# Kernel optimization log

Hardware: AMD Instinct MI355X
Metric: run time of the kernel (lower is better)

## Reference

```python
import jax, jax.numpy as jnp
import numpy as np

RCUT = 6.0
EPS = 1e-6
NUM_BASIS = 8
P = 6  # PolynomialSmooth envelope power
N_NODES = 100000
N_EDGES = 3200000
N_GRAPHS = 16

# 27 periodic image shifts: all integer combos of [-1,0,1]^3
_PERIODIC = jnp.asarray(
    np.stack(np.meshgrid(*([[-1, 0, 1]] * 3), indexing='ij'), -1).reshape(27, 3).astype(np.float32)
)


def _sh_lmax2(u):
    """e3nn spherical harmonics, lmax=2, normalize=True, normalization='component'.
    u: [E,3] unit vectors -> [E,9]."""
    x, y, z = u[..., 0], u[..., 1], u[..., 2]
    s3 = jnp.sqrt(jnp.asarray(3.0, u.dtype))
    s5 = jnp.sqrt(jnp.asarray(5.0, u.dtype))
    s15 = jnp.sqrt(jnp.asarray(15.0, u.dtype))
    return jnp.stack([
        jnp.ones_like(x),                      # l=0
        s3 * x, s3 * y, s3 * z,                # l=1
        s15 * x * z,                           # l=2
        s15 * x * y,
        s5 * (y * y - 0.5 * (x * x + z * z)),
        s15 * y * z,
        0.5 * s15 * (z * z - x * x),
    ], axis=-1)


def _bessel(lengths):
    # lengths: [E,1] -> [E,NUM_BASIS]
    k = jnp.arange(1, NUM_BASIS + 1, dtype=lengths.dtype) * jnp.pi / RCUT
    safe = jnp.clip(lengths, EPS, RCUT)
    return jnp.sin(safe * k) / (2.0 * safe)


def _poly_smooth(lengths):
    # standard polynomial envelope (DimeNet-style), zero at r=rcut
    x = jnp.clip(lengths / RCUT, 0.0, 1.0)
    c1 = (P + 1) * (P + 2) / 2.0
    c2 = float(P * (P + 2))
    c3 = P * (P + 1) / 2.0
    xp = x ** P
    return 1.0 - c1 * xp + c2 * xp * x - c3 * xp * x * x


def setup_inputs() -> dict:
    key = jax.random.key(0)
    k1, k2, k3, k4, k5 = jax.random.split(key, 5)
    pos = jax.random.normal(k1, (N_NODES, 3), dtype=jnp.float32) * 5.0
    cells = jax.random.normal(k2, (N_GRAPHS, 3, 3), dtype=jnp.float32)
    edge_index = jax.random.randint(k3, (2, N_EDGES), 0, N_NODES)
    periodic_index = jax.random.randint(k4, (N_EDGES,), 0, 27)
    batch = jnp.sort(jax.random.randint(k5, (N_NODES,), 0, N_GRAPHS))
    return {"pos": pos, "cells": cells, "edge_index": edge_index,
            "periodic_index": periodic_index, "batch": batch}


def reference(pos, cells, edge_index, periodic_index, batch):
    node_src, node_dst = edge_index[0], edge_index[1]
    vectors = pos[node_dst] - pos[node_src]                     # [E,3]
    shifts = _PERIODIC[periodic_index]                          # [E,3]
    src_cells = cells[batch[node_src]]                          # [E,3,3]
    vectors = vectors - jnp.einsum('eij,ei->ej', src_cells, shifts)
    vectors = -vectors                                          # dst == 'atom'
    lengths = jnp.linalg.norm(vectors, axis=-1, keepdims=True)  # [E,1]
    unit = vectors / jnp.maximum(lengths, EPS)                  # normalize=True
    attr = _sh_lmax2(unit)                                      # [E,9]
    basis = _bessel(lengths)                                    # [E,8]
    cutoff = _poly_smooth(lengths)                              # [E,1]
    basis_weight = basis * cutoff                               # [E,8]
    # pack (length, sh attr, smooth, basis_weight) -> [E,19]
    return jnp.concatenate([lengths, attr, cutoff, basis_weight], axis=-1)
```

## Files before the change

### kernel.cpp

```cpp
#include <hip/hip_runtime.h>

#define BLOCK 256
#define EPT 4
#define TILE (BLOCK * EPT)

typedef float vf4 __attribute__((ext_vector_type(4)));

extern "C" __global__ void __launch_bounds__(BLOCK) pack_pos_batch(
    const float* __restrict__ pos,
    const int*  __restrict__ batch,
    vf4* __restrict__ pos4,
    int N)
{
    const int i = blockIdx.x * BLOCK + threadIdx.x;
    if (i < N) {
        vf4 v;
        v.x = pos[3 * i + 0];
        v.y = pos[3 * i + 1];
        v.z = pos[3 * i + 2];
        v.w = __int_as_float(batch[i]);
        pos4[i] = v;
    }
}

template <bool PACKED>
__global__ void __launch_bounds__(BLOCK) edge_encoding_kernel(
    const float* __restrict__ pos,
    const vf4*   __restrict__ pos4,
    const float* __restrict__ cells,
    const int*   __restrict__ eidx,
    const int*   __restrict__ pidx,
    const int*   __restrict__ batch,
    float* __restrict__ out,
    int E)
{
    __shared__ vf4 s_t[16 * 27];
    __shared__ __align__(16) float s_out[BLOCK * 19];

    const int tid = threadIdx.x;
    for (int c = tid; c < 16 * 27; c += BLOCK) {
        const int g = c / 27, p = c % 27;
        const float f0 = (float)(p / 9 - 1);
        const float f1 = (float)((p / 3) % 3 - 1);
        const float f2 = (float)(p % 3 - 1);
        const float* C = cells + g * 9;
        vf4 t;
        t.x = C[0]*f0 + C[3]*f1 + C[6]*f2;
        t.y = C[1]*f0 + C[4]*f1 + C[7]*f2;
        t.z = C[2]*f0 + C[5]*f1 + C[8]*f2;
        t.w = 0.0f;
        s_t[c] = t;
    }
    __syncthreads();

    const long long b0 = (long long)blockIdx.x * TILE;

    int src[EPT], dst[EPT], pp[EPT];
    #pragma unroll
    for (int r = 0; r < EPT; ++r) {
        long long e = b0 + (long long)r * BLOCK + tid;
        if (e >= E) e = E - 1;
        src[r] = __builtin_nontemporal_load(eidx + e);
        dst[r] = __builtin_nontemporal_load(eidx + E + e);
        pp[r]  = __builtin_nontemporal_load(pidx + e);
    }
    vf4 ps[EPT], pd[EPT];
    #pragma unroll
    for (int r = 0; r < EPT; ++r) {
        if (PACKED) {
            ps[r] = pos4[src[r]];
            pd[r] = pos4[dst[r]];
        } else {
            const int s = src[r], d = dst[r];
            ps[r].x = pos[3*s+0]; ps[r].y = pos[3*s+1]; ps[r].z = pos[3*s+2];
            ps[r].w = __int_as_float(batch[s]);
            pd[r].x = pos[3*d+0]; pd[r].y = pos[3*d+1]; pd[r].z = pos[3*d+2];
            pd[r].w = 0.0f;
        }
    }

    const float s3  = 1.7320508075688772f;
    const float s5  = 2.2360679774997896f;
    const float s15 = 3.872983346207417f;

    #pragma unroll
    for (int c = 0; c < EPT; ++c) {
        float row[19];
        {
            const int g = __float_as_int(ps[c].w);
            const vf4 t = s_t[g * 27 + pp[c]];

            const float vx = ps[c].x - pd[c].x + t.x;
            const float vy = ps[c].y - pd[c].y + t.y;
            const float vz = ps[c].z - pd[c].z + t.z;

            const float len  = sqrtf(vx*vx + vy*vy + vz*vz);
            const float invl = __builtin_amdgcn_rcpf(fmaxf(len, 1e-6f));
            const float x = vx * invl, y = vy * invl, z = vz * invl;

            row[0] = len;
            row[1] = 1.0f;
            row[2] = s3 * x;
            row[3] = s3 * y;
            row[4] = s3 * z;
            row[5] = s15 * x * z;
            row[6] = s15 * x * y;
            row[7] = s5  * (y*y - 0.5f*(x*x + z*z));
            row[8] = s15 * y * z;
            row[9] = 0.5f * s15 * (z*z - x*x);

            const float xc = fminf(len * (1.0f/6.0f), 1.0f);
            const float x3 = xc * xc * xc;
            const float x6 = x3 * x3;
            const float cut = fmaf(x6, fmaf(xc, fmaf(-21.0f, xc, 48.0f), -28.0f), 1.0f);
            row[10] = cut;

            const float safe = fminf(fmaxf(len, 1e-6f), 6.0f);
            const float a = safe * 0.5235987755982988f;
            const float sa = __sinf(a);
            const float ca = __cosf(a);
            const float w = cut * 0.5f * __builtin_amdgcn_rcpf(safe);
            const float two_ca = 2.0f * ca;
            float s_prev = 0.0f, s_cur = sa;
            row[11] = s_cur * w;
            #pragma unroll
            for (int n = 2; n <= 8; ++n) {
                const float s_next = two_ca * s_cur - s_prev;
                s_prev = s_cur;
                s_cur  = s_next;
                row[10 + n] = s_cur * w;
            }
        }

        if (c > 0) __syncthreads();

        #pragma unroll
        for (int j = 0; j < 19; ++j) s_out[tid * 19 + j] = row[j];
        __syncthreads();

        const long long base_e = b0 + (long long)c * BLOCK;
        if (base_e < E) {
            const int nvalid  = (int)min((long long)BLOCK, (long long)E - base_e);
            const int nfloats = nvalid * 19;
            float* gout = out + base_e * 19;
            const int n4 = nfloats >> 2;
            const vf4* s4 = reinterpret_cast<const vf4*>(s_out);
            vf4* g4 = reinterpret_cast<vf4*>(gout);
            for (int i = tid; i < n4; i += BLOCK)
                g4[i] = s4[i];
            for (int i = (n4 << 2) + tid; i < nfloats; i += BLOCK)
                gout[i] = s_out[i];
        }
    }
}

extern "C" void kernel_launch(void* const* d_in, const int* in_sizes, int n_in,
                              void* d_out, int out_size, void* d_ws, size_t ws_size,
                              hipStream_t stream) {
    const float* pos   = (const float*)d_in[0];
    const float* cells = (const float*)d_in[1];
    const int*   eidx  = (const int*)d_in[2];
    const int*   pidx  = (const int*)d_in[3];
    const int*   batch = (const int*)d_in[4];
    float* out = (float*)d_out;

    const int E = in_sizes[3];
    const int N = in_sizes[4];
    const int grid = (int)(((long long)E + TILE - 1) / TILE);

    if (d_ws != nullptr && ws_size >= (size_t)N * sizeof(vf4)) {
        vf4* pos4 = (vf4*)d_ws;
        const int pgrid = (N + BLOCK - 1) / BLOCK;
        pack_pos_batch<<<pgrid, BLOCK, 0, stream>>>(pos, batch, pos4, N);
        edge_encoding_kernel<true><<<grid, BLOCK, 0, stream>>>(
            pos, pos4, cells, eidx, pidx, batch, out, E);
    } else {
        edge_encoding_kernel<false><<<grid, BLOCK, 0, stream>>>(
            pos, nullptr, cells, eidx, pidx, batch, out, E);
    }
}
```

Baseline: 321.8 us.

## Switch to per-wavefront edge tiles with private LDS staging and no block barriers

Each 64-lane wavefront now processes its own 64 edges and stages its output rows in a private LDS region before writing coalesced vf4 stores, removing block-wide __syncthreads. Per-thread work drops from four edges to one, and the grid grows accordingly. This aims to cut barrier stalls, at the cost of fewer outstanding gathers per thread. It also relies on implicit intra-wavefront ordering of LDS writes and reads.

Result: no change. 326.3 us (+1.4%).

```diff
diff --git a/kernel.cpp b/kernel.cpp
--- a/kernel.cpp
+++ b/kernel.cpp
@@ -1,8 +1,8 @@
 #include <hip/hip_runtime.h>
 
 #define BLOCK 256
-#define EPT 4
-#define TILE (BLOCK * EPT)
+#define WPB (BLOCK / 64)
+#define WREG (64 * 19)
 
 typedef float vf4 __attribute__((ext_vector_type(4)));
 
@@ -35,7 +35,7 @@
     int E)
 {
     __shared__ vf4 s_t[16 * 27];
-    __shared__ __align__(16) float s_out[BLOCK * 19];
+    __shared__ __align__(64) float s_out[WPB * WREG];
 
     const int tid = threadIdx.x;
     for (int c = tid; c < 16 * 27; c += BLOCK) {
@@ -53,104 +53,95 @@
     }
     __syncthreads();
 
-    const long long b0 = (long long)blockIdx.x * TILE;
+    const int lane = tid & 63;
+    const int wid  = tid >> 6;
+    const long long e0 = ((long long)blockIdx.x * WPB + wid) * 64;
+    if (e0 >= E) return;
 
-    int src[EPT], dst[EPT], pp[EPT];
-    #pragma unroll
-    for (int r = 0; r < EPT; ++r) {
-        long long e = b0 + (long long)r * BLOCK + tid;
-        if (e >= E) e = E - 1;
-        src[r] = __builtin_nontemporal_load(eidx + e);
-        dst[r] = __builtin_nontemporal_load(eidx + E + e);
-        pp[r]  = __builtin_nontemporal_load(pidx + e);
-    }
-    vf4 ps[EPT], pd[EPT];
-    #pragma unroll
-    for (int r = 0; r < EPT; ++r) {
-        if (PACKED) {
-            ps[r] = pos4[src[r]];
-            pd[r] = pos4[dst[r]];
-        } else {
-            const int s = src[r], d = dst[r];
-            ps[r].x = pos[3*s+0]; ps[r].y = pos[3*s+1]; ps[r].z = pos[3*s+2];
-            ps[r].w = __int_as_float(batch[s]);
-            pd[r].x = pos[3*d+0]; pd[r].y = pos[3*d+1]; pd[r].z = pos[3*d+2];
-            pd[r].w = 0.0f;
-        }
+    long long e = e0 + lane;
+    if (e >= E) e = E - 1;
+    const int src = __builtin_nontemporal_load(eidx + e);
+    const int dst = __builtin_nontemporal_load(eidx + E + e);
+    const int p   = __builtin_nontemporal_load(pidx + e);
+
+    vf4 ps, pd;
+    if (PACKED) {
+        ps = pos4[src];
+        pd = pos4[dst];
+    } else {
+        ps.x = pos[3*src+0]; ps.y = pos[3*src+1]; ps.z = pos[3*src+2];
+        ps.w = __int_as_float(batch[src]);
+        pd.x = pos[3*dst+0]; pd.y = pos[3*dst+1]; pd.z = pos[3*dst+2];
+        pd.w = 0.0f;
     }
 
     const float s3  = 1.7320508075688772f;
     const float s5  = 2.2360679774997896f;
     const float s15 = 3.872983346207417f;
 
+    float row[19];
+    {
+        const int g = __float_as_int(ps.w);
+        const vf4 t = s_t[g * 27 + p];
+
+        const float vx = ps.x - pd.x + t.x;
+        const float vy = ps.y - pd.y + t.y;
+        const float vz = ps.z - pd.z + t.z;
+
+        const float len  = sqrtf(vx*vx + vy*vy + vz*vz);
+        const float invl = __builtin_amdgcn_rcpf(fmaxf(len, 1e-6f));
+        const float x = vx * invl, y = vy * invl, z = vz * invl;
+
+        row[0] = len;
+        row[1] = 1.0f;
+        row[2] = s3 * x;
+        row[3] = s3 * y;
+        row[4] = s3 * z;
+        row[5] = s15 * x * z;
+        row[6] = s15 * x * y;
+        row[7] = s5  * (y*y - 0.5f*(x*x + z*z));
+        row[8] = s15 * y * z;
+        row[9] = 0.5f * s15 * (z*z - x*x);
+
+        const float xc = fminf(len * (1.0f/6.0f), 1.0f);
+        const float x3 = xc * xc * xc;
+        const float x6 = x3 * x3;
+        const float cut = fmaf(x6, fmaf(xc, fmaf(-21.0f, xc, 48.0f), -28.0f), 1.0f);
+        row[10] = cut;
+
+        const float safe = fminf(fmaxf(len, 1e-6f), 6.0f);
+        const float a = safe * 0.5235987755982988f;
+        const float sa = __sinf(a);
+        const float ca = __cosf(a);
+        const float w = cut * 0.5f * __builtin_amdgcn_rcpf(safe);
+        const float two_ca = 2.0f * ca;
+        float s_prev = 0.0f, s_cur = sa;
+        row[11] = s_cur * w;
+        #pragma unroll
+        for (int n = 2; n <= 8; ++n) {
+            const float s_next = two_ca * s_cur - s_prev;
+            s_prev = s_cur;
+            s_cur  = s_next;
+            row[10 + n] = s_cur * w;
+        }
+    }
+
+    float* s_buf = s_out + wid * WREG;
     #pragma unroll
-    for (int c = 0; c < EPT; ++c) {
-        float row[19];
-        {
-            const int g = __float_as_int(ps[c].w);
-            const vf4 t = s_t[g * 27 + pp[c]];
+    for (int j = 0; j < 19; ++j) s_buf[lane * 19 + j] = row[j];
 
-            const float vx = ps[c].x - pd[c].x + t.x;
-            const float vy = ps[c].y - pd[c].y + t.y;
-            const float vz = ps[c].z - pd[c].z + t.z;
-
-            const float len  = sqrtf(vx*vx + vy*vy + vz*vz);
-            const float invl = __builtin_amdgcn_rcpf(fmaxf(len, 1e-6f));
-            const float x = vx * invl, y = vy * invl, z = vz * invl;
-
-            row[0] = len;
-            row[1] = 1.0f;
-            row[2] = s3 * x;
-            row[3] = s3 * y;
-            row[4] = s3 * z;
-            row[5] = s15 * x * z;
-            row[6] = s15 * x * y;
-            row[7] = s5  * (y*y - 0.5f*(x*x + z*z));
-            row[8] = s15 * y * z;
-            row[9] = 0.5f * s15 * (z*z - x*x);
-
-            const float xc = fminf(len * (1.0f/6.0f), 1.0f);
-            const float x3 = xc * xc * xc;
-            const float x6 = x3 * x3;
-            const float cut = fmaf(x6, fmaf(xc, fmaf(-21.0f, xc, 48.0f), -28.0f), 1.0f);
-            row[10] = cut;
-
-            const float safe = fminf(fmaxf(len, 1e-6f), 6.0f);
-            const float a = safe * 0.5235987755982988f;
-            const float sa = __sinf(a);
-            const float ca = __cosf(a);
-            const float w = cut * 0.5f * __builtin_amdgcn_rcpf(safe);
-            const float two_ca = 2.0f * ca;
-            float s_prev = 0.0f, s_cur = sa;
-            row[11] = s_cur * w;
-            #pragma unroll
-            for (int n = 2; n <= 8; ++n) {
-                const float s_next = two_ca * s_cur - s_prev;
-                s_prev = s_cur;
-                s_cur  = s_next;
-                row[10 + n] = s_cur * w;
-            }
-        }
-
-        if (c > 0) __syncthreads();
-
+    const int nvalid = (int)(((long long)E - e0) < 64 ? (E - e0) : 64);
+    float* gout = out + e0 * 19;
+    if (nvalid == 64) {
+        const vf4* s4 = reinterpret_cast<const vf4*>(s_buf);
+        vf4* g4 = reinterpret_cast<vf4*>(gout);
         #pragma unroll
-        for (int j = 0; j < 19; ++j) s_out[tid * 19 + j] = row[j];
-        __syncthreads();
-
-        const long long base_e = b0 + (long long)c * BLOCK;
-        if (base_e < E) {
-            const int nvalid  = (int)min((long long)BLOCK, (long long)E - base_e);
-            const int nfloats = nvalid * 19;
-            float* gout = out + base_e * 19;
-            const int n4 = nfloats >> 2;
-            const vf4* s4 = reinterpret_cast<const vf4*>(s_out);
-            vf4* g4 = reinterpret_cast<vf4*>(gout);
-            for (int i = tid; i < n4; i += BLOCK)
-                g4[i] = s4[i];
-            for (int i = (n4 << 2) + tid; i < nfloats; i += BLOCK)
-                gout[i] = s_out[i];
-        }
+        for (int i = lane; i < 304; i += 64)
+            g4[i] = s4[i];
+    } else {
+        const int nf = nvalid * 19;
+        for (int i = lane; i < nf; i += 64)
+            gout[i] = s_buf[i];
     }
 }
 
@@ -166,7 +157,7 @@
 
     const int E = in_sizes[3];
     const int N = in_sizes[4];
-    const int grid = (int)(((long long)E + TILE - 1) / TILE);
+    const int grid = (int)(((long long)E + BLOCK - 1) / BLOCK);
 
     if (d_ws != nullptr && ws_size >= (size_t)N * sizeof(vf4)) {
         vf4* pos4 = (vf4*)d_ws;
```
